# Performance work log

Measured on AMD Instinct MI355X. Metric: run time of the kernel, lower is better.

## Reference

```python
import jax, jax.numpy as jnp
import numpy as np

N, D, T, E = 50000, 128, 6, 600000
LN_EPS = 1e-5


def setup_inputs() -> dict:
    key = jax.random.key(0)
    ks = jax.random.split(key, 8)
    x = jax.random.normal(ks[0], (N, D), dtype=jnp.float32)
    edge_index = jax.random.randint(ks[1], (2, E), 0, N, dtype=jnp.int64)
    edge_type = jax.random.randint(ks[2], (E,), 0, T, dtype=jnp.int64)
    s = 1.0 / np.sqrt(D)
    W_l = jax.random.normal(ks[3], (T, D, D), dtype=jnp.float32) * s
    W_r = jax.random.normal(ks[4], (T, D, D), dtype=jnp.float32) * s
    b = jax.random.normal(ks[5], (T, D), dtype=jnp.float32) * s
    emb = jax.random.normal(ks[6], (T, D), dtype=jnp.float32)
    gamma = jnp.ones((D,), dtype=jnp.float32)
    beta = jnp.zeros((D,), dtype=jnp.float32)
    return {"x": x, "edge_index": edge_index, "edge_type": edge_type,
            "W_l": W_l, "W_r": W_r, "b": b, "emb": emb,
            "gamma": gamma, "beta": beta}


def reference(x, edge_index, edge_type, W_l, W_r, b, emb, gamma, beta):
    n, d = x.shape
    t = W_l.shape[0]
    src, dst = edge_index[0], edge_index[1]
    # Combined segment id (dst, edge_type) -> one segment_sum for all types.
    seg = dst * t + edge_type
    msgs = x[src]  # (E, d) gathered source features
    sums = jax.ops.segment_sum(msgs, seg, num_segments=n * t).reshape(n, t, d)
    cnt = jax.ops.segment_sum(jnp.ones((seg.shape[0],), x.dtype), seg,
                              num_segments=n * t).reshape(n, t, 1)
    mean = sums / jnp.maximum(cnt, 1.0)  # PyG mean aggr: 0 for isolated nodes
    # Per-type SAGEConv: mean_t @ W_l[t] + x @ W_r[t] + b[t] + emb[t], summed over t.
    h = (jnp.einsum('ntd,tdo->no', mean, W_l)
         + x @ W_r.sum(0)
         + (b.sum(0) + emb.sum(0)))
    mu = jnp.mean(h, axis=-1, keepdims=True)
    var = jnp.var(h, axis=-1, keepdims=True)
    y = (h - mu) * jax.lax.rsqrt(var + LN_EPS) * gamma + beta
    return jax.nn.relu(y)
```

## Files before the change

### kernel.cpp

```cpp
#include <hip/hip_runtime.h>

#define TT 6
#define D 128
#define BM 64
#define CAP 1152
#define LN_EPS 1e-5f

typedef __bf16 bf16x8 __attribute__((ext_vector_type(8)));
typedef float f32x4 __attribute__((ext_vector_type(4)));

__device__ __forceinline__ unsigned short f2bf(float f) {
    unsigned int u = __float_as_uint(f);
    unsigned int r = (u + 0x7FFFu + ((u >> 16) & 1u)) >> 16;
    return (unsigned short)r;
}
__device__ __forceinline__ float bflo(unsigned int v) { return __uint_as_float(v << 16); }
__device__ __forceinline__ float bfhi(unsigned int v) { return __uint_as_float(v & 0xffff0000u); }

__device__ __forceinline__ int lds_off128(int row, int kgrp) {
    return row * 128 + (((kgrp & 7) ^ (row & 7)) | (kgrp & 8)) * 8;
}

__global__ void prep_kernel(const float* __restrict__ x, const float* __restrict__ W_l,
                            const float* __restrict__ W_r, const float* __restrict__ b,
                            const float* __restrict__ emb,
                            const int* __restrict__ ei, const int* __restrict__ et,
                            unsigned short* __restrict__ xb, unsigned short* __restrict__ WlT,
                            float* __restrict__ bias_total, int* __restrict__ bcursor,
                            int* __restrict__ ebuf,
                            int total8, int E, int N) {
    int i = blockIdx.x * 256 + threadIdx.x;
    if (i < total8) {
        const float4* p = (const float4*)x + (size_t)i * 2;
        float4 a = p[0], bb = p[1];
        uint4 o;
        o.x = (unsigned int)f2bf(a.x) | ((unsigned int)f2bf(a.y) << 16);
        o.y = (unsigned int)f2bf(a.z) | ((unsigned int)f2bf(a.w) << 16);
        o.z = (unsigned int)f2bf(bb.x) | ((unsigned int)f2bf(bb.y) << 16);
        o.w = (unsigned int)f2bf(bb.z) | ((unsigned int)f2bf(bb.w) << 16);
        ((uint4*)xb)[i] = o;
        return;
    }
    i -= total8;
    if (i < 7 * 2048) {
        int s = i >> 11, rem = i & 2047, kg = rem >> 7, n = rem & 127;
        float w[8];
        if (s < TT) {
#pragma unroll
            for (int j = 0; j < 8; ++j)
                w[j] = W_l[s * D * D + (kg * 8 + j) * D + n];
        } else {
#pragma unroll
            for (int j = 0; j < 8; ++j) {
                float sum = 0.f;
#pragma unroll
                for (int t = 0; t < TT; ++t)
                    sum += W_r[t * D * D + (kg * 8 + j) * D + n];
                w[j] = sum;
            }
        }
        uint4 o;
        o.x = (unsigned int)f2bf(w[0]) | ((unsigned int)f2bf(w[1]) << 16);
        o.y = (unsigned int)f2bf(w[2]) | ((unsigned int)f2bf(w[3]) << 16);
        o.z = (unsigned int)f2bf(w[4]) | ((unsigned int)f2bf(w[5]) << 16);
        o.w = (unsigned int)f2bf(w[6]) | ((unsigned int)f2bf(w[7]) << 16);
        *(uint4*)&WlT[(size_t)i * 8] = o;
        return;
    }
    i -= 7 * 2048;
    if (i < D) {
        float s = 0.f;
#pragma unroll
        for (int t = 0; t < TT; ++t) s += b[t * D + i] + emb[t * D + i];
        bias_total[i] = s;
        return;
    }
    i -= D;
    if (i < E) {
        int src = ei[i], dst = ei[E + i], t = et[i];
        int bkt = dst >> 6;
        int pos = atomicAdd(&bcursor[bkt * 16], 1);
        if (pos < CAP)
            ebuf[bkt * CAP + pos] = (src << 9) | ((dst & 63) << 3) | t;
    }
}

__launch_bounds__(256, 3)
__global__ void fused_kernel(const unsigned short* __restrict__ xb,
                             const int* __restrict__ bcursor, const int* __restrict__ ebuf,
                             const unsigned short* __restrict__ WlT,
                             const float* __restrict__ bias_total,
                             const float* __restrict__ gamma, const float* __restrict__ beta,
                             float* __restrict__ out, int N) {
    __shared__ unsigned short As[BM * 128];
    __shared__ int bcnt[TT * BM];
    __shared__ int bcur[TT * BM];
    __shared__ unsigned short esrt[CAP];

    int tid = threadIdx.x;
    int lane = tid & 63, wave = tid >> 6;
    int q = lane >> 4, c16 = lane & 15;
    int qid = tid >> 4, l16 = tid & 15;
    int blockRow = blockIdx.x * BM;

    int s0 = blockIdx.x * CAP;
    int bc = bcursor[blockIdx.x * 16];
    if (bc > CAP) bc = CAP;
#pragma unroll
    for (int j = 0; j < 2; ++j) {
        int idx = tid + j * 256;
        if (idx < TT * BM) { bcnt[idx] = 0; }
    }
    int pk0, pk1, pk2, pk3, pk4;
    {
        int e;
        e = tid;           pk0 = (e < bc) ? ebuf[s0 + e] : -1;
        e = tid + 256;     pk1 = (e < bc) ? ebuf[s0 + e] : -1;
        e = tid + 512;     pk2 = (e < bc) ? ebuf[s0 + e] : -1;
        e = tid + 768;     pk3 = (e < bc) ? ebuf[s0 + e] : -1;
        e = tid + 1024;    pk4 = (e < bc) ? ebuf[s0 + e] : -1;
    }
    __syncthreads();
    if (pk0 >= 0) atomicAdd(&bcnt[(pk0 & 7) * 64 + ((pk0 >> 3) & 63)], 1);
    if (pk1 >= 0) atomicAdd(&bcnt[(pk1 & 7) * 64 + ((pk1 >> 3) & 63)], 1);
    if (pk2 >= 0) atomicAdd(&bcnt[(pk2 & 7) * 64 + ((pk2 >> 3) & 63)], 1);
    if (pk3 >= 0) atomicAdd(&bcnt[(pk3 & 7) * 64 + ((pk3 >> 3) & 63)], 1);
    if (pk4 >= 0) atomicAdd(&bcnt[(pk4 & 7) * 64 + ((pk4 >> 3) & 63)], 1);
    __syncthreads();

    if (wave == 0) {
        int c[6];
        int ts = 0;
#pragma unroll
        for (int j = 0; j < 6; ++j) { c[j] = bcnt[lane * 6 + j]; ts += c[j]; }
        int inc = ts;
#pragma unroll
        for (int o = 1; o < 64; o <<= 1) {
            int n = __shfl_up(inc, o);
            if (lane >= o) inc += n;
        }
        int run = inc - ts;
#pragma unroll
        for (int j = 0; j < 6; ++j) { bcur[lane * 6 + j] = run; run += c[j]; }
    }
    __syncthreads();

    if (pk0 >= 0) { int s = (pk0 & 7) * 64 + ((pk0 >> 3) & 63); int p = atomicAdd(&bcur[s], 1); if (p < CAP) esrt[p] = (unsigned short)(pk0 >> 9); }
    if (pk1 >= 0) { int s = (pk1 & 7) * 64 + ((pk1 >> 3) & 63); int p = atomicAdd(&bcur[s], 1); if (p < CAP) esrt[p] = (unsigned short)(pk1 >> 9); }
    if (pk2 >= 0) { int s = (pk2 & 7) * 64 + ((pk2 >> 3) & 63); int p = atomicAdd(&bcur[s], 1); if (p < CAP) esrt[p] = (unsigned short)(pk2 >> 9); }
    if (pk3 >= 0) { int s = (pk3 & 7) * 64 + ((pk3 >> 3) & 63); int p = atomicAdd(&bcur[s], 1); if (p < CAP) esrt[p] = (unsigned short)(pk3 >> 9); }
    if (pk4 >= 0) { int s = (pk4 & 7) * 64 + ((pk4 >> 3) & 63); int p = atomicAdd(&bcur[s], 1); if (p < CAP) esrt[p] = (unsigned short)(pk4 >> 9); }
    __syncthreads();

    f32x4 acc[8];
#pragma unroll
    for (int ct = 0; ct < 8; ++ct) acc[ct] = (f32x4){0.f, 0.f, 0.f, 0.f};

    const unsigned short* Bbase = WlT + ((size_t)q * 128 + c16) * 8;

#pragma unroll 1
    for (int t = 0; t < 7; ++t) {
        bf16x8 afx[4];
        if (t < TT) {
#pragma unroll
            for (int pr = 0; pr < 2; ++pr) {
                int e0[2], cn[2];
#pragma unroll
                for (int i = 0; i < 2; ++i) {
                    int row = qid * 4 + pr * 2 + i;
                    int s = t * 64 + row;
                    int c = bcnt[s];
                    cn[i] = c;
                    e0[i] = bcur[s] - c;
                }
                int ix[2][4];
#pragma unroll
                for (int i = 0; i < 2; ++i)
#pragma unroll
                    for (int j = 0; j < 4; ++j)
                        ix[i][j] = (cn[i] > j) ? (int)esrt[e0[i] + j] : 0;
                uint4 v[2][4];
#pragma unroll
                for (int i = 0; i < 2; ++i)
#pragma unroll
                    for (int j = 0; j < 4; ++j) {
                        v[i][j] = (uint4){0u, 0u, 0u, 0u};
                        if (cn[i] > j)
                            v[i][j] = *(const uint4*)(xb + (size_t)ix[i][j] * D + l16 * 8);
                    }
#pragma unroll
                for (int i = 0; i < 2; ++i) {
                    float a0 = bflo(v[i][0].x) + bflo(v[i][1].x) + bflo(v[i][2].x) + bflo(v[i][3].x);
                    float a1 = bfhi(v[i][0].x) + bfhi(v[i][1].x) + bfhi(v[i][2].x) + bfhi(v[i][3].x);
                    float a2 = bflo(v[i][0].y) + bflo(v[i][1].y) + bflo(v[i][2].y) + bflo(v[i][3].y);
                    float a3 = bfhi(v[i][0].y) + bfhi(v[i][1].y) + bfhi(v[i][2].y) + bfhi(v[i][3].y);
                    float a4 = bflo(v[i][0].z) + bflo(v[i][1].z) + bflo(v[i][2].z) + bflo(v[i][3].z);
                    float a5 = bfhi(v[i][0].z) + bfhi(v[i][1].z) + bfhi(v[i][2].z) + bfhi(v[i][3].z);
                    float a6 = bflo(v[i][0].w) + bflo(v[i][1].w) + bflo(v[i][2].w) + bflo(v[i][3].w);
                    float a7 = bfhi(v[i][0].w) + bfhi(v[i][1].w) + bfhi(v[i][2].w) + bfhi(v[i][3].w);
                    int e = e0[i] + 4, end = e0[i] + cn[i];
#pragma unroll 1
                    while (e < end) {
                        int s = (int)esrt[e++];
                        uint4 vv = *(const uint4*)(xb + (size_t)s * D + l16 * 8);
                        a0 += bflo(vv.x); a1 += bfhi(vv.x);
                        a2 += bflo(vv.y); a3 += bfhi(vv.y);
                        a4 += bflo(vv.z); a5 += bfhi(vv.z);
                        a6 += bflo(vv.w); a7 += bfhi(vv.w);
                    }
                    if (cn[i] > 1) {
                        float sc = 1.f / (float)cn[i];
                        a0 *= sc; a1 *= sc; a2 *= sc; a3 *= sc;
                        a4 *= sc; a5 *= sc; a6 *= sc; a7 *= sc;
                    }
                    uint4 p;
                    p.x = (unsigned int)f2bf(a0) | ((unsigned int)f2bf(a1) << 16);
                    p.y = (unsigned int)f2bf(a2) | ((unsigned int)f2bf(a3) << 16);
                    p.z = (unsigned int)f2bf(a4) | ((unsigned int)f2bf(a5) << 16);
                    p.w = (unsigned int)f2bf(a6) | ((unsigned int)f2bf(a7) << 16);
                    *(uint4*)&As[lds_off128(qid * 4 + pr * 2 + i, l16)] = p;
                }
            }
        } else {
            int gr = blockRow + wave * 16 + c16; if (gr >= N) gr = N - 1;
#pragma unroll
            for (int ks = 0; ks < 4; ++ks)
                afx[ks] = *(const bf16x8*)(xb + (size_t)gr * D + (ks * 4 + q) * 8);
        }

        const unsigned short* Bt = Bbase + (size_t)t * 16384;
#pragma unroll
        for (int ks = 0; ks < 4; ++ks) {
            bf16x8 af;
            if (t < TT)
                af = *(const bf16x8*)&As[lds_off128(wave * 16 + c16, ks * 4 + q)];
            else
                af = afx[ks];
#pragma unroll
            for (int ct = 0; ct < 8; ++ct) {
                bf16x8 bfr = *(const bf16x8*)(Bt + ks * 4096 + ct * 128);
                acc[ct] = __builtin_amdgcn_mfma_f32_16x16x32_bf16(af, bfr, acc[ct], 0, 0, 0);
            }
        }
    }

    float bias_c[8], g_c[8], bt_c[8];
#pragma unroll
    for (int ct = 0; ct < 8; ++ct) {
        int col = ct * 16 + c16;
        bias_c[ct] = bias_total[col];
        g_c[ct] = gamma[col];
        bt_c[ct] = beta[col];
    }
#pragma unroll
    for (int reg = 0; reg < 4; ++reg) {
        float h[8];
        float s = 0.f, s2 = 0.f;
#pragma unroll
        for (int ct = 0; ct < 8; ++ct) {
            h[ct] = acc[ct][reg] + bias_c[ct];
            s += h[ct];
            s2 += h[ct] * h[ct];
        }
#pragma unroll
        for (int o = 8; o >= 1; o >>= 1) {
            s  += __shfl_xor(s, o, 16);
            s2 += __shfl_xor(s2, o, 16);
        }
        float mu = s * (1.f / 128.f);
        float var = s2 * (1.f / 128.f) - mu * mu;
        float rstd = rsqrtf(var + LN_EPS);
        int row = blockRow + wave * 16 + q * 4 + reg;
        if (row < N) {
#pragma unroll
            for (int ct = 0; ct < 8; ++ct) {
                float y = (h[ct] - mu) * rstd * g_c[ct] + bt_c[ct];
                out[(size_t)row * D + ct * 16 + c16] = fmaxf(y, 0.f);
            }
        }
    }
}

extern "C" void kernel_launch(void* const* d_in, const int* in_sizes, int n_in,
                              void* d_out, int out_size, void* d_ws, size_t ws_size,
                              hipStream_t stream) {
    const float* x     = (const float*)d_in[0];
    const int*   ei    = (const int*)d_in[1];
    const int*   et    = (const int*)d_in[2];
    const float* W_l   = (const float*)d_in[3];
    const float* W_r   = (const float*)d_in[4];
    const float* b     = (const float*)d_in[5];
    const float* emb   = (const float*)d_in[6];
    const float* gamma = (const float*)d_in[7];
    const float* beta  = (const float*)d_in[8];

    int N = in_sizes[0] / D;
    int E = in_sizes[2];
    int NBLK = (N + BM - 1) / BM;

    int* bcursor = (int*)d_ws;
    int* ebuf    = bcursor + NBLK * 16;
    size_t ofs = (size_t)((char*)(ebuf + (size_t)NBLK * CAP) - (char*)d_ws);
    ofs = (ofs + 15) & ~(size_t)15;
    unsigned short* WlT = (unsigned short*)((char*)d_ws + ofs);
    float* bias_total = (float*)(WlT + 7 * 2048 * 8);
    size_t ofs2 = (size_t)((char*)(bias_total + D) - (char*)d_ws);
    ofs2 = (ofs2 + 15) & ~(size_t)15;
    unsigned short* xb = (unsigned short*)((char*)d_ws + ofs2);

    hipMemsetAsync(bcursor, 0, (size_t)(NBLK * 16) * sizeof(int), stream);

    int total8 = N * D / 8;
    int G = total8 + 7 * 2048 + D + E;
    prep_kernel<<<(G + 255) / 256, 256, 0, stream>>>(x, W_l, W_r, b, emb, ei, et,
                                                     xb, WlT, bias_total, bcursor, ebuf,
                                                     total8, E, N);

    fused_kernel<<<NBLK, 256, 0, stream>>>(xb, bcursor, ebuf, WlT, bias_total,
                                           gamma, beta, (float*)d_out, N);
}
```

Measured before the change: 189.1 us.

## Bucket edges via block-local LDS counting sort before global scatter

The edge bucketing in the prep kernel moves from one global atomicAdd per edge to a per-block counting sort in LDS over 8192-edge chunks. Each chunk then reserves space with one global atomic per bucket and writes contiguous runs into ebuf. This cuts global atomic contention and makes the writes coalesced, but adds LDS use and several syncs to the prep blocks. Separately, the gather stage in the fused kernel now issues loads for all four rows at once instead of two pairs, which raises memory-level parallelism at the cost of more registers.

```diff
diff --git a/kernel.cpp b/kernel.cpp
--- a/kernel.cpp
+++ b/kernel.cpp
@@ -4,6 +4,8 @@
 #define D 128
 #define BM 64
 #define CAP 1152
+#define NBKT 782
+#define FILLT 8192
 #define LN_EPS 1e-5f
 
 typedef __bf16 bf16x8 __attribute__((ext_vector_type(8)));
@@ -28,8 +30,84 @@
                             unsigned short* __restrict__ xb, unsigned short* __restrict__ WlT,
                             float* __restrict__ bias_total, int* __restrict__ bcursor,
                             int* __restrict__ ebuf,
-                            int total8, int E, int N) {
-    int i = blockIdx.x * 256 + threadIdx.x;
+                            int total8, int E, int N, int FILLB) {
+    __shared__ int srt[FILLT];
+    __shared__ int lcnt[1024];
+    __shared__ int lbase[1024];
+    __shared__ int lpos[1024];
+    __shared__ int gbase[1024];
+    __shared__ int wsum[4];
+    __shared__ int woff[4];
+
+    int tid = threadIdx.x;
+    if (blockIdx.x < (unsigned)FILLB) {
+        int lane = tid & 63, wave = tid >> 6;
+        int e0 = blockIdx.x * FILLT;
+#pragma unroll
+        for (int j = 0; j < 4; ++j) lcnt[tid * 4 + j] = 0;
+        __syncthreads();
+#pragma unroll 1
+        for (int j = 0; j < FILLT / 256; ++j) {
+            int e = e0 + j * 256 + tid;
+            if (e < E) atomicAdd(&lcnt[ei[E + e] >> 6], 1);
+        }
+        __syncthreads();
+        int c[4];
+        int ts = 0;
+#pragma unroll
+        for (int j = 0; j < 4; ++j) { c[j] = lcnt[tid * 4 + j]; ts += c[j]; }
+        int inc = ts;
+#pragma unroll
+        for (int o = 1; o < 64; o <<= 1) {
+            int n = __shfl_up(inc, o);
+            if (lane >= o) inc += n;
+        }
+        if (lane == 63) wsum[wave] = inc;
+        __syncthreads();
+        if (tid == 0) {
+            int r = 0;
+#pragma unroll
+            for (int w = 0; w < 4; ++w) { int t = wsum[w]; woff[w] = r; r += t; }
+        }
+        __syncthreads();
+        int run = woff[wave] + inc - ts;
+#pragma unroll
+        for (int j = 0; j < 4; ++j) {
+            int idx = tid * 4 + j;
+            lbase[idx] = run; lpos[idx] = run;
+            run += c[j];
+        }
+        __syncthreads();
+#pragma unroll 1
+        for (int j = 0; j < FILLT / 256; ++j) {
+            int e = e0 + j * 256 + tid;
+            if (e < E) {
+                int src = ei[e], dst = ei[E + e], t = et[e];
+                int bkt = dst >> 6;
+                int pk = (src << 9) | ((dst & 63) << 3) | t;
+                int p = atomicAdd(&lpos[bkt], 1);
+                srt[p] = pk;
+            }
+        }
+        __syncthreads();
+        for (int bk = tid; bk < NBKT; bk += 256) {
+            int cnt = lpos[bk] - lbase[bk];
+            gbase[bk] = (cnt > 0) ? atomicAdd(&bcursor[bk * 16], cnt) : 0;
+        }
+        __syncthreads();
+        for (int bk = wave; bk < NBKT; bk += 4) {
+            int lb = lbase[bk];
+            int cnt = lpos[bk] - lb;
+            int gb = gbase[bk];
+            for (int k = lane; k < cnt; k += 64) {
+                int gpos = gb + k;
+                if (gpos < CAP) ebuf[bk * CAP + gpos] = srt[lb + k];
+            }
+        }
+        return;
+    }
+
+    int i = (blockIdx.x - FILLB) * 256 + tid;
     if (i < total8) {
         const float4* p = (const float4*)x + (size_t)i * 2;
         float4 a = p[0], bb = p[1];
@@ -73,15 +151,6 @@
 #pragma unroll
         for (int t = 0; t < TT; ++t) s += b[t * D + i] + emb[t * D + i];
         bias_total[i] = s;
-        return;
-    }
-    i -= D;
-    if (i < E) {
-        int src = ei[i], dst = ei[E + i], t = et[i];
-        int bkt = dst >> 6;
-        int pos = atomicAdd(&bcursor[bkt * 16], 1);
-        if (pos < CAP)
-            ebuf[bkt * CAP + pos] = (src << 9) | ((dst & 63) << 3) | t;
     }
 }
 
@@ -162,64 +231,61 @@
     for (int t = 0; t < 7; ++t) {
         bf16x8 afx[4];
         if (t < TT) {
-#pragma unroll
-            for (int pr = 0; pr < 2; ++pr) {
-                int e0[2], cn[2];
-#pragma unroll
-                for (int i = 0; i < 2; ++i) {
-                    int row = qid * 4 + pr * 2 + i;
-                    int s = t * 64 + row;
-                    int c = bcnt[s];
-                    cn[i] = c;
-                    e0[i] = bcur[s] - c;
+            int e0[4], cn[4];
+#pragma unroll
+            for (int i = 0; i < 4; ++i) {
+                int row = qid * 4 + i;
+                int s = t * 64 + row;
+                int c = bcnt[s];
+                cn[i] = c;
+                e0[i] = bcur[s] - c;
+            }
+            int ix[4][4];
+#pragma unroll
+            for (int i = 0; i < 4; ++i)
+#pragma unroll
+                for (int j = 0; j < 4; ++j)
+                    ix[i][j] = (cn[i] > j) ? (int)esrt[e0[i] + j] : 0;
+            uint4 v[4][4];
+#pragma unroll
+            for (int i = 0; i < 4; ++i)
+#pragma unroll
+                for (int j = 0; j < 4; ++j) {
+                    v[i][j] = (uint4){0u, 0u, 0u, 0u};
+                    if (cn[i] > j)
+                        v[i][j] = *(const uint4*)(xb + (size_t)ix[i][j] * D + l16 * 8);
                 }
-                int ix[2][4];
-#pragma unroll
-                for (int i = 0; i < 2; ++i)
-#pragma unroll
-                    for (int j = 0; j < 4; ++j)
-                        ix[i][j] = (cn[i] > j) ? (int)esrt[e0[i] + j] : 0;
-                uint4 v[2][4];
-#pragma unroll
-                for (int i = 0; i < 2; ++i)
-#pragma unroll
-                    for (int j = 0; j < 4; ++j) {
-                        v[i][j] = (uint4){0u, 0u, 0u, 0u};
-                        if (cn[i] > j)
-                            v[i][j] = *(const uint4*)(xb + (size_t)ix[i][j] * D + l16 * 8);
-                    }
-#pragma unroll
-                for (int i = 0; i < 2; ++i) {
-                    float a0 = bflo(v[i][0].x) + bflo(v[i][1].x) + bflo(v[i][2].x) + bflo(v[i][3].x);
-                    float a1 = bfhi(v[i][0].x) + bfhi(v[i][1].x) + bfhi(v[i][2].x) + bfhi(v[i][3].x);
-                    float a2 = bflo(v[i][0].y) + bflo(v[i][1].y) + bflo(v[i][2].y) + bflo(v[i][3].y);
-                    float a3 = bfhi(v[i][0].y) + bfhi(v[i][1].y) + bfhi(v[i][2].y) + bfhi(v[i][3].y);
-                    float a4 = bflo(v[i][0].z) + bflo(v[i][1].z) + bflo(v[i][2].z) + bflo(v[i][3].z);
-                    float a5 = bfhi(v[i][0].z) + bfhi(v[i][1].z) + bfhi(v[i][2].z) + bfhi(v[i][3].z);
-                    float a6 = bflo(v[i][0].w) + bflo(v[i][1].w) + bflo(v[i][2].w) + bflo(v[i][3].w);
-                    float a7 = bfhi(v[i][0].w) + bfhi(v[i][1].w) + bfhi(v[i][2].w) + bfhi(v[i][3].w);
-                    int e = e0[i] + 4, end = e0[i] + cn[i];
+#pragma unroll
+            for (int i = 0; i < 4; ++i) {
+                float a0 = bflo(v[i][0].x) + bflo(v[i][1].x) + bflo(v[i][2].x) + bflo(v[i][3].x);
+                float a1 = bfhi(v[i][0].x) + bfhi(v[i][1].x) + bfhi(v[i][2].x) + bfhi(v[i][3].x);
+                float a2 = bflo(v[i][0].y) + bflo(v[i][1].y) + bflo(v[i][2].y) + bflo(v[i][3].y);
+                float a3 = bfhi(v[i][0].y) + bfhi(v[i][1].y) + bfhi(v[i][2].y) + bfhi(v[i][3].y);
+                float a4 = bflo(v[i][0].z) + bflo(v[i][1].z) + bflo(v[i][2].z) + bflo(v[i][3].z);
+                float a5 = bfhi(v[i][0].z) + bfhi(v[i][1].z) + bfhi(v[i][2].z) + bfhi(v[i][3].z);
+                float a6 = bflo(v[i][0].w) + bflo(v[i][1].w) + bflo(v[i][2].w) + bflo(v[i][3].w);
+                float a7 = bfhi(v[i][0].w) + bfhi(v[i][1].w) + bfhi(v[i][2].w) + bfhi(v[i][3].w);
+                int e = e0[i] + 4, end = e0[i] + cn[i];
 #pragma unroll 1
-                    while (e < end) {
-                        int s = (int)esrt[e++];
-                        uint4 vv = *(const uint4*)(xb + (size_t)s * D + l16 * 8);
-                        a0 += bflo(vv.x); a1 += bfhi(vv.x);
-                        a2 += bflo(vv.y); a3 += bfhi(vv.y);
-                        a4 += bflo(vv.z); a5 += bfhi(vv.z);
-                        a6 += bflo(vv.w); a7 += bfhi(vv.w);
-                    }
-                    if (cn[i] > 1) {
-                        float sc = 1.f / (float)cn[i];
-                        a0 *= sc; a1 *= sc; a2 *= sc; a3 *= sc;
-                        a4 *= sc; a5 *= sc; a6 *= sc; a7 *= sc;
-                    }
-                    uint4 p;
-                    p.x = (unsigned int)f2bf(a0) | ((unsigned int)f2bf(a1) << 16);
-                    p.y = (unsigned int)f2bf(a2) | ((unsigned int)f2bf(a3) << 16);
-                    p.z = (unsigned int)f2bf(a4) | ((unsigned int)f2bf(a5) << 16);
-                    p.w = (unsigned int)f2bf(a6) | ((unsigned int)f2bf(a7) << 16);
-                    *(uint4*)&As[lds_off128(qid * 4 + pr * 2 + i, l16)] = p;
+                while (e < end) {
+                    int s = (int)esrt[e++];
+                    uint4 vv = *(const uint4*)(xb + (size_t)s * D + l16 * 8);
+                    a0 += bflo(vv.x); a1 += bfhi(vv.x);
+                    a2 += bflo(vv.y); a3 += bfhi(vv.y);
+                    a4 += bflo(vv.z); a5 += bfhi(vv.z);
+                    a6 += bflo(vv.w); a7 += bfhi(vv.w);
                 }
+                if (cn[i] > 1) {
+                    float sc = 1.f / (float)cn[i];
+                    a0 *= sc; a1 *= sc; a2 *= sc; a3 *= sc;
+                    a4 *= sc; a5 *= sc; a6 *= sc; a7 *= sc;
+                }
+                uint4 p;
+                p.x = (unsigned int)f2bf(a0) | ((unsigned int)f2bf(a1) << 16);
+                p.y = (unsigned int)f2bf(a2) | ((unsigned int)f2bf(a3) << 16);
+                p.z = (unsigned int)f2bf(a4) | ((unsigned int)f2bf(a5) << 16);
+                p.w = (unsigned int)f2bf(a6) | ((unsigned int)f2bf(a7) << 16);
+                *(uint4*)&As[lds_off128(qid * 4 + i, l16)] = p;
             }
         } else {
             int gr = blockRow + wave * 16 + c16; if (gr >= N) gr = N - 1;
@@ -311,10 +377,12 @@
     hipMemsetAsync(bcursor, 0, (size_t)(NBLK * 16) * sizeof(int), stream);
 
     int total8 = N * D / 8;
-    int G = total8 + 7 * 2048 + D + E;
-    prep_kernel<<<(G + 255) / 256, 256, 0, stream>>>(x, W_l, W_r, b, emb, ei, et,
-                                                     xb, WlT, bias_total, bcursor, ebuf,
-                                                     total8, E, N);
+    int FILLB = (E + FILLT - 1) / FILLT;
+    int G2 = total8 + 7 * 2048 + D;
+    int GRID = FILLB + (G2 + 255) / 256;
+    prep_kernel<<<GRID, 256, 0, stream>>>(x, W_l, W_r, b, emb, ei, et,
+                                          xb, WlT, bias_total, bcursor, ebuf,
+                                          total8, E, N, FILLB);
 
     fused_kernel<<<NBLK, 256, 0, stream>>>(xb, bcursor, ebuf, WlT, bias_total,
                                            gamma, beta, (float*)d_out, N);
```

Measured after the change: 242.8 us. +28.3%, slower.
